# Performance work log

Hardware: AMD Instinct MI355X
Metric: run time of the kernel (lower is better)

## Reference

```python
import jax, jax.numpy as jnp
import numpy as np

FP4_MAX = 6.0
FP8_MAX = 448.0  # float8_e4m3fn max
BLOCK = 16
# representable |values| of fp4 e2m1 and decision midpoints (ties round up)
FP4_LEVELS = jnp.array([0.0, 0.5, 1.0, 1.5, 2.0, 3.0, 4.0, 6.0], dtype=jnp.float32)
FP4_MIDS = jnp.array([0.25, 0.75, 1.25, 1.75, 2.5, 3.5, 5.0], dtype=jnp.float32)


def _fp4_round(x):
    # round to nearest fp4 e2m1 value (magnitudes clamp at 6)
    a = jnp.abs(x)
    idx = jnp.searchsorted(FP4_MIDS, a, side='right')
    return jnp.sign(x) * FP4_LEVELS[idx]


def nvfp4_quant(x, global_scale):
    # x: [M, K] float32 -> (q_fp4 values [M, K], block scales [M, K//16] fp8-representable)
    M, K = x.shape
    xb = x.reshape(M, K // BLOCK, BLOCK)
    block_amax = jnp.max(jnp.abs(xb), axis=-1)  # [M, K//16]
    scale = jnp.clip(block_amax * (global_scale / FP4_MAX), 0.0, FP8_MAX)
    scale = scale.astype(jnp.float8_e4m3fn).astype(jnp.float32)
    safe = jnp.where(scale == 0.0, 1.0, scale)
    q = _fp4_round(xb * (global_scale / safe)[..., None])
    return q.reshape(M, K), scale


def setup_inputs() -> dict:
    key = jax.random.key(0)
    k_in, k_w, k_b = jax.random.split(key, 3)
    M, K, N = 256, 5120, 13824
    x = jax.random.normal(k_in, (M, K), dtype=jnp.float32)
    # build pre-quantized NVFP4 weight buffers (as the module's load_quantized_weights would)
    w = jax.random.normal(k_w, (N, K), dtype=jnp.float32) * 0.02
    w_gs = (FP8_MAX * FP4_MAX) / jnp.max(jnp.abs(w))  # scalar float32
    w_fp4, w_scale = nvfp4_quant(w, w_gs)
    bias = jax.random.normal(k_b, (N,), dtype=jnp.float32) * 0.01
    return {
        'input': x,
        'weight_fp4': w_fp4,            # [N, K] fp4 values held in f32
        'weight_scale': w_scale,        # [N, K//16] fp8_e4m3-representable f32
        'weight_global_scale': w_gs,    # scalar f32
        'bias': bias,                   # [N]
    }


def reference(input, weight_fp4, weight_scale, weight_global_scale, bias):
    # activations cast to bf16 (as in the torch module), math in f32
    x = input.astype(jnp.bfloat16).astype(jnp.float32)
    M, K = x.shape
    N = weight_fp4.shape[0]
    # per-tensor global scale for activations
    a_gs = (FP8_MAX * FP4_MAX) / jnp.max(jnp.abs(x))
    alpha = 1.0 / (a_gs * weight_global_scale)
    # on-the-fly fp4 quantization of activations
    a_fp4, a_scale = nvfp4_quant(x, a_gs)
    # block-scaled dequant-matmul: out = (a_fp4*s_a) @ (w_fp4*s_w)^T * alpha + bias
    a_u = (a_fp4.reshape(M, K // BLOCK, BLOCK) * a_scale[..., None]).reshape(M, K)
    w_u = (weight_fp4.reshape(N, K // BLOCK, BLOCK) * weight_scale[..., None]).reshape(N, K)
    out = jnp.einsum('mk,nk->mn', a_u, w_u) * alpha + bias[None, :]
    return out
```

## Files before the change

kernel.cpp:

```cpp
#include <hip/hip_runtime.h>

typedef __attribute__((ext_vector_type(8))) __bf16 bf16x8;
typedef __attribute__((ext_vector_type(4))) __bf16 bf16x4;
typedef __attribute__((ext_vector_type(4))) float floatx4;

#define M_TOT 256
#define K_TOT 5120
#define N_TOT 13824
#define NBLK  320
#define BN    64
#define BK    32
#define KSPLIT 4
#define KCH   1280
#define NSTEP 40

#define GLOAD_LDS16(g, l)                                                     \
  __builtin_amdgcn_global_load_lds(                                           \
      (const __attribute__((address_space(1))) void*)(g),                     \
      (__attribute__((address_space(3))) void*)(l), 16, 0, 0)

static __device__ __forceinline__ float bf16r(float v) { return (float)(__bf16)v; }

static __device__ __forceinline__ float fp4round(float v) {
  float a = fabsf(v), q;
  if      (a < 0.25f) q = 0.0f;
  else if (a < 0.75f) q = 0.5f;
  else if (a < 1.25f) q = 1.0f;
  else if (a < 1.75f) q = 1.5f;
  else if (a < 2.5f)  q = 2.0f;
  else if (a < 3.5f)  q = 3.0f;
  else if (a < 5.0f)  q = 4.0f;
  else                q = 6.0f;
  return copysignf(q, v);
}

static __device__ __forceinline__ float cvt_e4m3(float f) {
  if (f < 0.015625f) return rintf(f * 512.0f) * 0.001953125f;
  int e = (int)(__float_as_uint(f) >> 23) - 127;
  float q = __uint_as_float((unsigned)(e - 3 + 127) << 23);
  return rintf(f / q) * q;
}

__global__ void k_prep(const float* __restrict__ x, unsigned* __restrict__ amax_bits,
                       float4* __restrict__ out4) {
  int idx = blockIdx.x * blockDim.x + threadIdx.x;
#pragma unroll 1
  for (int j = idx; j < 884736; j += 327680) out4[j] = (float4){0.f, 0.f, 0.f, 0.f};
  float4 v = ((const float4*)x)[idx];
  float m = fmaxf(fmaxf(fabsf(bf16r(v.x)), fabsf(bf16r(v.y))),
                  fmaxf(fabsf(bf16r(v.z)), fabsf(bf16r(v.w))));
#pragma unroll
  for (int off = 32; off; off >>= 1) m = fmaxf(m, __shfl_xor(m, off));
  if ((threadIdx.x & 63) == 0) atomicMax(amax_bits, __float_as_uint(m));
}

__global__ void k_aquant(const float* __restrict__ x,
                         const unsigned* __restrict__ amax_bits,
                         __bf16* __restrict__ au) {
  int idx = blockIdx.x * blockDim.x + threadIdx.x;
  int m = idx / NBLK;
  int b = idx - m * NBLK;
  float amax = __uint_as_float(*amax_bits);
  float gs  = 2688.0f / amax;
  float gs6 = gs / 6.0f;
  const float4* xp = (const float4*)(x + m * K_TOT + b * 16);
  float4 v0 = xp[0], v1 = xp[1], v2 = xp[2], v3 = xp[3];
  float xv[16];
  xv[0]=bf16r(v0.x); xv[1]=bf16r(v0.y); xv[2]=bf16r(v0.z); xv[3]=bf16r(v0.w);
  xv[4]=bf16r(v1.x); xv[5]=bf16r(v1.y); xv[6]=bf16r(v1.z); xv[7]=bf16r(v1.w);
  xv[8]=bf16r(v2.x); xv[9]=bf16r(v2.y); xv[10]=bf16r(v2.z); xv[11]=bf16r(v2.w);
  xv[12]=bf16r(v3.x); xv[13]=bf16r(v3.y); xv[14]=bf16r(v3.z); xv[15]=bf16r(v3.w);
  float am = 0.f;
#pragma unroll
  for (int j = 0; j < 16; ++j) am = fmaxf(am, fabsf(xv[j]));
  float s = cvt_e4m3(fminf(am * gs6, 448.0f));
  float g = gs / ((s == 0.f) ? 1.f : s);
  bf16x8 p0, p1;
#pragma unroll
  for (int j = 0; j < 8; ++j) p0[j] = (__bf16)(fp4round(xv[j] * g) * s);
#pragma unroll
  for (int j = 0; j < 8; ++j) p1[j] = (__bf16)(fp4round(xv[8 + j] * g) * s);
  bf16x8* dst = (bf16x8*)(au + (size_t)idx * 16);
  dst[0] = p0; dst[1] = p1;
}

__global__ __launch_bounds__(512, 4) void k_gemm(
    const __bf16* __restrict__ au,
    const float*  __restrict__ w,
    const float*  __restrict__ wsc,
    const unsigned* __restrict__ amax_bits,
    const float*  __restrict__ wgs,
    const float*  __restrict__ bias,
    float* __restrict__ out)
{
  __shared__ __bf16 Ab[4][M_TOT * BK];
  __shared__ __bf16 Bb[4][BN * BK];

  const int tid  = threadIdx.x;
  const int lane = tid & 63;
  const int wv   = tid >> 6;
  const int wm   = wv >> 1;
  const int wn   = wv & 1;

  const int s     = blockIdx.x & (KSPLIT - 1);
  const int n0    = (blockIdx.x >> 2) * BN;
  const int kbase = s * KCH;

  const int arow  = wv * 32 + (lane >> 2);
  const int acolp = 8 * ((lane & 3) ^ ((lane >> 3) & 3));

  const int brow = tid >> 3;
  const int bcg  = tid & 7;
  const float* wp  = w   + (size_t)(n0 + brow) * K_TOT + kbase + bcg * 4;
  const float* wsp = wsc + (size_t)(n0 + brow) * NBLK + s * (KCH / 16);
  const int bsci = bcg >> 2;
  const int bdst = brow * 64 + (((bcg >> 1) ^ ((brow >> 1) & 3)) << 4) + (bcg & 1) * 8;

  const int hi  = lane >> 4;
  const int r15 = lane & 15;
  const int rsw = (r15 >> 1) & 3;

  floatx4 acc[4][2];
#pragma unroll
  for (int fm = 0; fm < 4; ++fm)
#pragma unroll
    for (int fn = 0; fn < 2; ++fn) acc[fm][fn] = (floatx4){0.f, 0.f, 0.f, 0.f};

  auto issueA = [&](int t, int slot) {
    const __bf16* src = au + (size_t)arow * K_TOT + kbase + t * BK + acolp;
    char* dst = (char*)(&Ab[slot][0]) + wv * 2048;
    GLOAD_LDS16(src, dst);
    GLOAD_LDS16(src + (size_t)16 * K_TOT, dst + 1024);
  };
  auto writeB = [&](float4 bv, float bs, int slot) {
    bf16x4 pk;
    pk[0] = (__bf16)(bv.x * bs); pk[1] = (__bf16)(bv.y * bs);
    pk[2] = (__bf16)(bv.z * bs); pk[3] = (__bf16)(bv.w * bs);
    *(bf16x4*)((char*)(&Bb[slot][0]) + bdst) = pk;
  };
  auto compute = [&](int slot) {
    char* pA = (char*)(&Ab[slot][0]);
    char* pB = (char*)(&Bb[slot][0]);
    bf16x8 af[4], bfr[2];
#pragma unroll
    for (int fm = 0; fm < 4; ++fm) {
      const int row = wm * 64 + fm * 16 + r15;
      af[fm] = *(const bf16x8*)(pA + row * 64 + ((hi ^ rsw) << 4));
    }
#pragma unroll
    for (int fn = 0; fn < 2; ++fn) {
      const int row = wn * 32 + fn * 16 + r15;
      bfr[fn] = *(const bf16x8*)(pB + row * 64 + ((hi ^ rsw) << 4));
    }
#pragma unroll
    for (int fm = 0; fm < 4; ++fm)
#pragma unroll
      for (int fn = 0; fn < 2; ++fn)
        acc[fm][fn] = __builtin_amdgcn_mfma_f32_16x16x32_bf16(af[fm], bfr[fn], acc[fm][fn], 0, 0, 0);
  };

  float4 bvA, bvB; float bsA, bsB;

  issueA(0, 0);
  bvA = *(const float4*)(wp);          bsA = wsp[bsci];
  issueA(1, 1);
  bvB = *(const float4*)(wp + BK);     bsB = wsp[2 + bsci];
  asm volatile("s_waitcnt vmcnt(4)" ::: "memory");
  writeB(bvA, bsA, 0);

#pragma unroll 1
  for (int t = 0; t < NSTEP; t += 2) {
    if (t + 2 < NSTEP) {
      issueA(t + 2, (t + 2) & 3);
      bvA = *(const float4*)(wp + (t + 2) * BK);
      bsA = wsp[(t + 2) * 2 + bsci];
      asm volatile("s_waitcnt vmcnt(4)" ::: "memory");
    } else {
      asm volatile("s_waitcnt vmcnt(0)" ::: "memory");
    }
    writeB(bvB, bsB, (t + 1) & 3);
    asm volatile("s_waitcnt lgkmcnt(0)" ::: "memory");
    __builtin_amdgcn_sched_barrier(0);
    __builtin_amdgcn_s_barrier();
    __builtin_amdgcn_sched_barrier(0);
    compute(t & 3);

    if (t + 3 < NSTEP) {
      issueA(t + 3, (t + 3) & 3);
      bvB = *(const float4*)(wp + (t + 3) * BK);
      bsB = wsp[(t + 3) * 2 + bsci];
      asm volatile("s_waitcnt vmcnt(4)" ::: "memory");
      writeB(bvA, bsA, (t + 2) & 3);
    } else if (t + 2 < NSTEP) {
      asm volatile("s_waitcnt vmcnt(0)" ::: "memory");
      writeB(bvA, bsA, (t + 2) & 3);
    }
    asm volatile("s_waitcnt lgkmcnt(0)" ::: "memory");
    __builtin_amdgcn_sched_barrier(0);
    __builtin_amdgcn_s_barrier();
    __builtin_amdgcn_sched_barrier(0);
    compute((t + 1) & 3);
  }

  float amax = __uint_as_float(*amax_bits);
  float a_gs = 2688.0f / amax;
  float alpha = 1.0f / (a_gs * wgs[0]);
#pragma unroll
  for (int fm = 0; fm < 4; ++fm) {
#pragma unroll
    for (int fn = 0; fn < 2; ++fn) {
      int mrow = wm * 64 + fm * 16 + hi * 4;
      int ncol = n0 + wn * 32 + fn * 16 + r15;
      float bb = (s == 0) ? bias[ncol] : 0.0f;
#pragma unroll
      for (int j = 0; j < 4; ++j)
        atomicAdd(&out[(size_t)(mrow + j) * N_TOT + ncol],
                  acc[fm][fn][j] * alpha + bb);
    }
  }
}

extern "C" void kernel_launch(void* const* d_in, const int* in_sizes, int n_in,
                              void* d_out, int out_size, void* d_ws, size_t ws_size,
                              hipStream_t stream) {
  const float* x    = (const float*)d_in[0];
  const float* wq   = (const float*)d_in[1];
  const float* wsc  = (const float*)d_in[2];
  const float* wgs  = (const float*)d_in[3];
  const float* bias = (const float*)d_in[4];
  float* out = (float*)d_out;

  unsigned* amax = (unsigned*)d_ws;
  __bf16* au = (__bf16*)((char*)d_ws + 256);

  hipMemsetAsync(d_ws, 0, 4, stream);
  k_prep<<<dim3(1280), dim3(256), 0, stream>>>(x, amax, (float4*)out);
  k_aquant<<<dim3(M_TOT * NBLK / 256), dim3(256), 0, stream>>>(x, amax, au);
  k_gemm<<<dim3((N_TOT / BN) * KSPLIT), dim3(512), 0, stream>>>(au, wq, wsc, amax, wgs, bias, out);
}
```

Measured before the change: 237.3 us.

## Restructure GEMM: 1024-thread blocks, BN=128, weights fed directly to registers

Result: slower. 248.2 us (+4.6%).

```diff
diff --git a/kernel.cpp b/kernel.cpp
--- a/kernel.cpp
+++ b/kernel.cpp
@@ -1,18 +1,17 @@
 #include <hip/hip_runtime.h>
 
 typedef __attribute__((ext_vector_type(8))) __bf16 bf16x8;
-typedef __attribute__((ext_vector_type(4))) __bf16 bf16x4;
 typedef __attribute__((ext_vector_type(4))) float floatx4;
 
 #define M_TOT 256
 #define K_TOT 5120
 #define N_TOT 13824
 #define NBLK  320
-#define BN    64
-#define BK    32
+#define BN    128
 #define KSPLIT 4
 #define KCH   1280
-#define NSTEP 40
+#define KSUP  256
+#define NSUP  5
 
 #define GLOAD_LDS16(g, l)                                                     \
   __builtin_amdgcn_global_load_lds(                                           \
@@ -84,7 +83,7 @@
   dst[0] = p0; dst[1] = p1;
 }
 
-__global__ __launch_bounds__(512, 4) void k_gemm(
+__global__ __launch_bounds__(1024, 4) void k_gemm(
     const __bf16* __restrict__ au,
     const float*  __restrict__ w,
     const float*  __restrict__ wsc,
@@ -93,130 +92,118 @@
     const float*  __restrict__ bias,
     float* __restrict__ out)
 {
-  __shared__ __bf16 Ab[4][M_TOT * BK];
-  __shared__ __bf16 Bb[4][BN * BK];
+  __shared__ __bf16 Ab[M_TOT * KSUP];
 
   const int tid  = threadIdx.x;
   const int lane = tid & 63;
   const int wv   = tid >> 6;
-  const int wm   = wv >> 1;
-  const int wn   = wv & 1;
-
-  const int s     = blockIdx.x & (KSPLIT - 1);
+  const int wm   = wv >> 3;
+  const int wn   = wv & 7;
+
+  const int s     = blockIdx.x & 3;
   const int n0    = (blockIdx.x >> 2) * BN;
   const int kbase = s * KCH;
 
-  const int arow  = wv * 32 + (lane >> 2);
-  const int acolp = 8 * ((lane & 3) ^ ((lane >> 3) & 3));
-
-  const int brow = tid >> 3;
-  const int bcg  = tid & 7;
-  const float* wp  = w   + (size_t)(n0 + brow) * K_TOT + kbase + bcg * 4;
-  const float* wsp = wsc + (size_t)(n0 + brow) * NBLK + s * (KCH / 16);
-  const int bsci = bcg >> 2;
-  const int bdst = brow * 64 + (((bcg >> 1) ^ ((brow >> 1) & 3)) << 4) + (bcg & 1) * 8;
-
   const int hi  = lane >> 4;
   const int r15 = lane & 15;
-  const int rsw = (r15 >> 1) & 3;
-
-  floatx4 acc[4][2];
-#pragma unroll
-  for (int fm = 0; fm < 4; ++fm)
-#pragma unroll
-    for (int fn = 0; fn < 2; ++fn) acc[fm][fn] = (floatx4){0.f, 0.f, 0.f, 0.f};
-
-  auto issueA = [&](int t, int slot) {
-    const __bf16* src = au + (size_t)arow * K_TOT + kbase + t * BK + acolp;
-    char* dst = (char*)(&Ab[slot][0]) + wv * 2048;
-    GLOAD_LDS16(src, dst);
-    GLOAD_LDS16(src + (size_t)16 * K_TOT, dst + 1024);
-  };
-  auto writeB = [&](float4 bv, float bs, int slot) {
-    bf16x4 pk;
-    pk[0] = (__bf16)(bv.x * bs); pk[1] = (__bf16)(bv.y * bs);
-    pk[2] = (__bf16)(bv.z * bs); pk[3] = (__bf16)(bv.w * bs);
-    *(bf16x4*)((char*)(&Bb[slot][0]) + bdst) = pk;
-  };
-  auto compute = [&](int slot) {
-    char* pA = (char*)(&Ab[slot][0]);
-    char* pB = (char*)(&Bb[slot][0]);
-    bf16x8 af[4], bfr[2];
-#pragma unroll
-    for (int fm = 0; fm < 4; ++fm) {
-      const int row = wm * 64 + fm * 16 + r15;
-      af[fm] = *(const bf16x8*)(pA + row * 64 + ((hi ^ rsw) << 4));
+  const int xo  = r15 & 7;
+
+  const int arow0 = tid >> 5;
+  const int achk  = (tid & 31) ^ ((tid >> 5) & 7);
+  const __bf16* asrc0 = au + (size_t)arow0 * K_TOT + kbase + achk * 8;
+
+  const int nrow = n0 + wn * 16 + r15;
+  const float* wrow  = w   + (size_t)nrow * K_TOT + kbase + hi * 8;
+  const float* wsrow = wsc + (size_t)nrow * NBLK + s * (KCH / 16);
+  const int hi2 = hi >> 1;
+
+  const int abase = (wm * 128 + r15) * 512;
+  const int cof0  = ((0 * 4 + hi) ^ xo) << 4;
+  const int cof1  = ((1 * 4 + hi) ^ xo) << 4;
+
+  floatx4 acc[8];
+#pragma unroll
+  for (int fm = 0; fm < 8; ++fm) acc[fm] = (floatx4){0.f, 0.f, 0.f, 0.f};
+
+  struct WSlot { float4 a, b, c, d; float s0, s1; };
+  WSlot sA, sB;
+
+  auto issueA = [&](int c) {
+    const __bf16* src = asrc0 + c * KSUP;
+    char* dst = (char*)Ab + tid * 16;
+#pragma unroll
+    for (int i = 0; i < 8; ++i)
+      GLOAD_LDS16(src + (size_t)i * 32 * K_TOT, dst + i * 16384);
+  };
+  auto issueW = [&](WSlot& sl, int t) {
+    const float* p = wrow + t * 64;
+    sl.a = *(const float4*)(p);
+    sl.b = *(const float4*)(p + 4);
+    sl.c = *(const float4*)(p + 32);
+    sl.d = *(const float4*)(p + 36);
+    sl.s0 = wsrow[t * 4 + hi2];
+    sl.s1 = wsrow[t * 4 + 2 + hi2];
+  };
+  auto cvt8 = [](float4 x, float4 y, float sc) {
+    bf16x8 r;
+    r[0] = (__bf16)(x.x * sc); r[1] = (__bf16)(x.y * sc);
+    r[2] = (__bf16)(x.z * sc); r[3] = (__bf16)(x.w * sc);
+    r[4] = (__bf16)(y.x * sc); r[5] = (__bf16)(y.y * sc);
+    r[6] = (__bf16)(y.z * sc); r[7] = (__bf16)(y.w * sc);
+    return r;
+  };
+  auto stepC = [&](WSlot& sl, int j, int tre) {
+    bf16x8 b0 = cvt8(sl.a, sl.b, sl.s0);
+    bf16x8 b1 = cvt8(sl.c, sl.d, sl.s1);
+    if (tre >= 0) issueW(sl, tre);
+    const char* pA = (const char*)Ab + abase + j * 128;
+#pragma unroll
+    for (int fm = 0; fm < 8; ++fm) {
+      bf16x8 af = *(const bf16x8*)(pA + fm * 8192 + cof0);
+      acc[fm] = __builtin_amdgcn_mfma_f32_16x16x32_bf16(af, b0, acc[fm], 0, 0, 0);
     }
 #pragma unroll
-    for (int fn = 0; fn < 2; ++fn) {
-      const int row = wn * 32 + fn * 16 + r15;
-      bfr[fn] = *(const bf16x8*)(pB + row * 64 + ((hi ^ rsw) << 4));
+    for (int fm = 0; fm < 8; ++fm) {
+      bf16x8 af = *(const bf16x8*)(pA + fm * 8192 + cof1);
+      acc[fm] = __builtin_amdgcn_mfma_f32_16x16x32_bf16(af, b1, acc[fm], 0, 0, 0);
     }
-#pragma unroll
-    for (int fm = 0; fm < 4; ++fm)
-#pragma unroll
-      for (int fn = 0; fn < 2; ++fn)
-        acc[fm][fn] = __builtin_amdgcn_mfma_f32_16x16x32_bf16(af[fm], bfr[fn], acc[fm][fn], 0, 0, 0);
-  };
-
-  float4 bvA, bvB; float bsA, bsB;
-
-  issueA(0, 0);
-  bvA = *(const float4*)(wp);          bsA = wsp[bsci];
-  issueA(1, 1);
-  bvB = *(const float4*)(wp + BK);     bsB = wsp[2 + bsci];
-  asm volatile("s_waitcnt vmcnt(4)" ::: "memory");
-  writeB(bvA, bsA, 0);
+  };
 
 #pragma unroll 1
-  for (int t = 0; t < NSTEP; t += 2) {
-    if (t + 2 < NSTEP) {
-      issueA(t + 2, (t + 2) & 3);
-      bvA = *(const float4*)(wp + (t + 2) * BK);
-      bsA = wsp[(t + 2) * 2 + bsci];
-      asm volatile("s_waitcnt vmcnt(4)" ::: "memory");
-    } else {
-      asm volatile("s_waitcnt vmcnt(0)" ::: "memory");
+  for (int c = 0; c < NSUP; ++c) {
+    const int tb = c * 4;
+    if (c > 0) {
+      asm volatile("s_waitcnt lgkmcnt(0)" ::: "memory");
+      __builtin_amdgcn_sched_barrier(0);
+      __builtin_amdgcn_s_barrier();
+      __builtin_amdgcn_sched_barrier(0);
     }
-    writeB(bvB, bsB, (t + 1) & 3);
-    asm volatile("s_waitcnt lgkmcnt(0)" ::: "memory");
+    issueA(c);
+    __builtin_amdgcn_sched_barrier(0);
+    issueW(sA, tb + 0);
+    issueW(sB, tb + 1);
+    asm volatile("s_waitcnt vmcnt(8)" ::: "memory");
     __builtin_amdgcn_sched_barrier(0);
     __builtin_amdgcn_s_barrier();
     __builtin_amdgcn_sched_barrier(0);
-    compute(t & 3);
-
-    if (t + 3 < NSTEP) {
-      issueA(t + 3, (t + 3) & 3);
-      bvB = *(const float4*)(wp + (t + 3) * BK);
-      bsB = wsp[(t + 3) * 2 + bsci];
-      asm volatile("s_waitcnt vmcnt(4)" ::: "memory");
-      writeB(bvA, bsA, (t + 2) & 3);
-    } else if (t + 2 < NSTEP) {
-      asm volatile("s_waitcnt vmcnt(0)" ::: "memory");
-      writeB(bvA, bsA, (t + 2) & 3);
-    }
-    asm volatile("s_waitcnt lgkmcnt(0)" ::: "memory");
-    __builtin_amdgcn_sched_barrier(0);
-    __builtin_amdgcn_s_barrier();
-    __builtin_amdgcn_sched_barrier(0);
-    compute((t + 1) & 3);
+    stepC(sA, 0, tb + 2);
+    stepC(sB, 1, tb + 3);
+    stepC(sA, 2, -1);
+    stepC(sB, 3, -1);
   }
 
   float amax = __uint_as_float(*amax_bits);
   float a_gs = 2688.0f / amax;
   float alpha = 1.0f / (a_gs * wgs[0]);
-#pragma unroll
-  for (int fm = 0; fm < 4; ++fm) {
-#pragma unroll
-    for (int fn = 0; fn < 2; ++fn) {
-      int mrow = wm * 64 + fm * 16 + hi * 4;
-      int ncol = n0 + wn * 32 + fn * 16 + r15;
-      float bb = (s == 0) ? bias[ncol] : 0.0f;
-#pragma unroll
-      for (int j = 0; j < 4; ++j)
-        atomicAdd(&out[(size_t)(mrow + j) * N_TOT + ncol],
-                  acc[fm][fn][j] * alpha + bb);
-    }
+  const int ncol = n0 + wn * 16 + r15;
+  const float bb = (s == 0) ? bias[ncol] : 0.0f;
+#pragma unroll
+  for (int fm = 0; fm < 8; ++fm) {
+    int mrow = wm * 128 + fm * 16 + hi * 4;
+#pragma unroll
+    for (int j = 0; j < 4; ++j)
+      atomicAdd(&out[(size_t)(mrow + j) * N_TOT + ncol],
+                acc[fm][j] * alpha + bb);
   }
 }
 
@@ -236,5 +223,5 @@
   hipMemsetAsync(d_ws, 0, 4, stream);
   k_prep<<<dim3(1280), dim3(256), 0, stream>>>(x, amax, (float4*)out);
   k_aquant<<<dim3(M_TOT * NBLK / 256), dim3(256), 0, stream>>>(x, amax, au);
-  k_gemm<<<dim3((N_TOT / BN) * KSPLIT), dim3(512), 0, stream>>>(au, wq, wsc, amax, wgs, bias, out);
-}
+  k_gemm<<<dim3((N_TOT / BN) * KSPLIT), dim3(1024), 0, stream>>>(au, wq, wsc, amax, wgs, bias, out);
+}
```
